# Kernel tuning notes

Hardware: AMD Instinct MI355X
Metric: run time of the kernel (lower is better)

## Reference

```python
import jax, jax.numpy as jnp
from jax import lax
import numpy as np

B, T, I, H, C = 32, 256, 128, 128, 100


def setup_inputs() -> dict:
    key = jax.random.key(0)
    ks = jax.random.split(key, 9)
    s = 1.0 / np.sqrt(H)  # PyTorch LSTMCell init range
    inp = {
        "x": jax.random.normal(ks[0], (B, T, I), dtype=jnp.float32),
        "w_ih": jax.random.uniform(ks[1], (4 * H, I), jnp.float32, -s, s),
        "b_ih": jax.random.uniform(ks[2], (4 * H,), jnp.float32, -s, s),
        "w_hh": jax.random.uniform(ks[3], (4 * H, H), jnp.float32, -s, s),
        "b_hh": jax.random.uniform(ks[4], (4 * H,), jnp.float32, -s, s),
        # attention params: normal(mean=0, std=0.01) per the source
        "w1": 0.01 * jax.random.normal(ks[5], (2 * H, H), dtype=jnp.float32),
        "w2": 0.01 * jax.random.normal(ks[6], (H, 1), dtype=jnp.float32),
        "w_fc": jax.random.uniform(ks[7], (C, H), jnp.float32, -s, s),
        "b_fc": jax.random.uniform(ks[8], (C,), jnp.float32, -s, s),
    }
    return inp


def _forward(x, w_ih, b_ih, w_hh, b_hh, w1, w2, w_fc, b_fc):
    Bv, Tv, _ = x.shape
    Hv = w_hh.shape[1]
    h0 = jnp.zeros((Bv, Hv), x.dtype)
    c0 = jnp.zeros((Bv, Hv), x.dtype)
    # memory buffer: slot 0 holds the initial zero hidden state (as in the
    # torch code, h_old starts as h_t=0); slots 1..T filled as we go.
    # Unwritten (future) slots are zero, so their attn contribution
    # attn_w * h_old is exactly zero -> no mask needed, matching the
    # growing-memory semantics of the original loop.
    mem0 = jnp.zeros((Bv, Tv + 1, Hv), x.dtype)
    attn0 = jnp.zeros((Bv, Hv), x.dtype)

    def step(carry, inp):
        h, c, mem, _ = carry
        x_t, i = inp
        # PyTorch LSTMCell: gate order i, f, g, o
        gates = x_t @ w_ih.T + b_ih + h @ w_hh.T + b_hh
        ig, fg, gg, og = jnp.split(gates, 4, axis=-1)
        c = jax.nn.sigmoid(fg) * c + jax.nn.sigmoid(ig) * jnp.tanh(gg)
        h = jax.nn.sigmoid(og) * jnp.tanh(c)
        # additive attention scores over the memory (NO softmax in source)
        h_rep = jnp.broadcast_to(h[:, None, :], mem.shape)  # [B, T+1, H]
        cat = jnp.concatenate([h_rep, mem], axis=-1)        # [B, T+1, 2H]
        s = jnp.tanh(cat @ w1) @ w2                          # [B, T+1, 1]
        attn_c = jnp.sum(s * mem, axis=1)                    # [B, H]
        mem = mem.at[:, i + 1, :].set(h)  # append h_t to memory
        return (h, c, mem, attn_c), None

    xs = (jnp.transpose(x, (1, 0, 2)), jnp.arange(Tv))
    (h, c, mem, attn_c), _ = lax.scan(step, (h0, c0, mem0, attn0), xs)
    return (h + attn_c) @ w_fc.T + b_fc


def reference(x, w_ih, b_ih, w_hh, b_hh, w1, w2, w_fc, b_fc):
    return _forward(x, w_ih, b_ih, w_hh, b_hh, w1, w2, w_fc, b_fc)
```

## Files before the change

kernel.cpp:

```cpp
#include <hip/hip_runtime.h>
#include <hip/hip_bf16.h>


#define Bsz 32
#define Tsz 256
#define Isz 128
#define Hsz 128
#define Csz 100
#define G4H 512

__device__ __forceinline__ float2 pk_fma(float2 a, float2 b, float2 c) {
    float2 d;
    asm("v_pk_fma_f32 %0, %1, %2, %3" : "=v"(d) : "v"(a), "v"(b), "v"(c));
    return d;
}
__device__ __forceinline__ float quad_rsum(float x) {
    int t = __builtin_amdgcn_update_dpp(0, __float_as_int(x), 0xB1, 0xF, 0xF, true);
    x += __int_as_float(t);
    t = __builtin_amdgcn_update_dpp(0, __float_as_int(x), 0x4E, 0xF, 0xF, true);
    x += __int_as_float(t);
    return x;
}
__device__ __forceinline__ float rcpf(float x) { return __builtin_amdgcn_rcpf(x); }
__device__ __forceinline__ float sigm_n(float x) { return rcpf(1.0f + __expf(-x)); }
__device__ __forceinline__ float tanh_n(float x) {
    float ax = fabsf(x);
    float e = __expf(-2.0f * ax);
    float t = (1.0f - e) * rcpf(1.0f + e);
    return copysignf(t, x);
}
__device__ __forceinline__ float tanh_s(float x) { return tanh_n(x); }

__global__ __launch_bounds__(256) void prep_kernel(
    const float* __restrict__ w_ih, const float* __restrict__ b_ih,
    const float* __restrict__ w_hh, const float* __restrict__ b_hh,
    float* __restrict__ wih_t, float* __restrict__ whh_pk, float* __restrict__ bias) {
    int idx = blockIdx.x * blockDim.x + threadIdx.x;
    if (idx < G4H * Isz) {
        int j = idx >> 7;
        int k = idx & 127;
        wih_t[k * G4H + j] = w_ih[idx];

        int j4  = idx & 3;
        int q   = (idx >> 2) & 3;
        int d   = (idx >> 4) & 127;
        int gi  = (idx >> 11) & 3;
        int kk4 = (idx >> 13) & 7;
        whh_pk[idx] = w_hh[(size_t)((gi << 7) + d) * 128 + (q << 5) + (kk4 << 2) + j4];
    }
    if (idx < G4H) bias[idx] = b_ih[idx] + b_hh[idx];
}

#define GBK 16
#define GLD 132

__global__ __launch_bounds__(256) void gemm128(
    const float* __restrict__ A, const float* __restrict__ Bm,
    const float* __restrict__ bias, float* __restrict__ C,
    int M, int N, int K) {
    __shared__ float As[GBK][GLD];
    __shared__ float Bs[GBK][GLD];
    const int tid = threadIdx.x;
    const int bm = blockIdx.y * 128;
    const int bn = blockIdx.x * 128;
    const int tx = tid & 15, ty = tid >> 4;
    float acc[8][8] = {};

    const int ar = tid >> 2;
    const int ac = (tid & 3) * 4;
    const int br = tid >> 5;
    const int bc = (tid & 31) * 4;

    for (int k0 = 0; k0 < K; k0 += GBK) {
        #pragma unroll
        for (int h = 0; h < 2; ++h) {
            int r = ar + 64 * h;
            float4 v = *(const float4*)(A + (size_t)(bm + r) * K + k0 + ac);
            As[ac + 0][r] = v.x;
            As[ac + 1][r] = v.y;
            As[ac + 2][r] = v.z;
            As[ac + 3][r] = v.w;
        }
        #pragma unroll
        for (int h = 0; h < 2; ++h) {
            int kr = br + 8 * h;
            float4 v = *(const float4*)(Bm + (size_t)(k0 + kr) * N + bn + bc);
            *(float4*)&Bs[kr][bc] = v;
        }
        __syncthreads();
        #pragma unroll
        for (int kk = 0; kk < GBK; ++kk) {
            float a[8], b[8];
            *(float4*)&a[0] = *(const float4*)&As[kk][ty * 8];
            *(float4*)&a[4] = *(const float4*)&As[kk][ty * 8 + 4];
            *(float4*)&b[0] = *(const float4*)&Bs[kk][tx * 8];
            *(float4*)&b[4] = *(const float4*)&Bs[kk][tx * 8 + 4];
            #pragma unroll
            for (int i = 0; i < 8; ++i)
                #pragma unroll
                for (int j = 0; j < 8; ++j)
                    acc[i][j] = fmaf(a[i], b[j], acc[i][j]);
        }
        __syncthreads();
    }
    float bb[8];
    #pragma unroll
    for (int j = 0; j < 8; ++j) bb[j] = bias ? bias[bn + tx * 8 + j] : 0.0f;
    #pragma unroll
    for (int i = 0; i < 8; ++i) {
        int row = bm + ty * 8 + i;
        float4 v0, v1;
        v0.x = acc[i][0] + bb[0]; v0.y = acc[i][1] + bb[1];
        v0.z = acc[i][2] + bb[2]; v0.w = acc[i][3] + bb[3];
        v1.x = acc[i][4] + bb[4]; v1.y = acc[i][5] + bb[5];
        v1.z = acc[i][6] + bb[6]; v1.w = acc[i][7] + bb[7];
        *(float4*)(C + (size_t)row * N + bn + tx * 8) = v0;
        *(float4*)(C + (size_t)row * N + bn + tx * 8 + 4) = v1;
    }
}

#define BM 64
#define BN 64
#define BKt 64
#define LDP 68

__global__ __launch_bounds__(256) void gemm_tn(
    const float* __restrict__ A, const float* __restrict__ Bm,
    const float* __restrict__ bias, float* __restrict__ C,
    int M, int N, int K) {
    __shared__ float As[BKt][LDP];
    __shared__ float Bs[BKt][LDP];
    int tid = threadIdx.x;
    int bm = blockIdx.y * BM;
    int bn = blockIdx.x * BN;
    int tx = tid & 15, ty = tid >> 4;
    float acc[4][4] = {};

    int lr = tid >> 4;
    int lc = (tid & 15) * 4;

    for (int k0 = 0; k0 < K; k0 += BKt) {
        #pragma unroll
        for (int p = 0; p < 4; ++p) {
            int row = p * 16 + lr;
            float4 v = *(const float4*)(A + (size_t)(bm + row) * K + k0 + lc);
            As[lc + 0][row] = v.x;
            As[lc + 1][row] = v.y;
            As[lc + 2][row] = v.z;
            As[lc + 3][row] = v.w;
        }
        #pragma unroll
        for (int p = 0; p < 4; ++p) {
            int kr = p * 16 + lr;
            float4 v = *(const float4*)(Bm + (size_t)(k0 + kr) * N + bn + lc);
            *(float4*)&Bs[kr][lc] = v;
        }
        __syncthreads();
        #pragma unroll
        for (int kk = 0; kk < BKt; ++kk) {
            float4 a = *(const float4*)&As[kk][ty * 4];
            float4 b = *(const float4*)&Bs[kk][tx * 4];
            acc[0][0] = fmaf(a.x, b.x, acc[0][0]);
            acc[0][1] = fmaf(a.x, b.y, acc[0][1]);
            acc[0][2] = fmaf(a.x, b.z, acc[0][2]);
            acc[0][3] = fmaf(a.x, b.w, acc[0][3]);
            acc[1][0] = fmaf(a.y, b.x, acc[1][0]);
            acc[1][1] = fmaf(a.y, b.y, acc[1][1]);
            acc[1][2] = fmaf(a.y, b.z, acc[1][2]);
            acc[1][3] = fmaf(a.y, b.w, acc[1][3]);
            acc[2][0] = fmaf(a.z, b.x, acc[2][0]);
            acc[2][1] = fmaf(a.z, b.y, acc[2][1]);
            acc[2][2] = fmaf(a.z, b.z, acc[2][2]);
            acc[2][3] = fmaf(a.z, b.w, acc[2][3]);
            acc[3][0] = fmaf(a.w, b.x, acc[3][0]);
            acc[3][1] = fmaf(a.w, b.y, acc[3][1]);
            acc[3][2] = fmaf(a.w, b.z, acc[3][2]);
            acc[3][3] = fmaf(a.w, b.w, acc[3][3]);
        }
        __syncthreads();
    }
    float bb[4] = {0.f, 0.f, 0.f, 0.f};
    if (bias) {
        bb[0] = bias[bn + tx * 4 + 0];
        bb[1] = bias[bn + tx * 4 + 1];
        bb[2] = bias[bn + tx * 4 + 2];
        bb[3] = bias[bn + tx * 4 + 3];
    }
    #pragma unroll
    for (int i = 0; i < 4; ++i) {
        int row = bm + ty * 4 + i;
        float4 v;
        v.x = acc[i][0] + bb[0];
        v.y = acc[i][1] + bb[1];
        v.z = acc[i][2] + bb[2];
        v.w = acc[i][3] + bb[3];
        *(float4*)(C + (size_t)row * N + bn + tx * 4) = v;
    }
}

#define HPAD(k) ((k) + 8 * ((k) >> 5))

__global__ __launch_bounds__(512, 2) void lstm_seq(
    const float* __restrict__ G, const float* __restrict__ whh_pk,
    float* __restrict__ H_all) {
    const int b = blockIdx.x;
    const int tid = threadIdx.x;
    const int d = tid >> 2;
    const int q = tid & 3;

    __shared__ float h_s[2][160];
    __shared__ float ring[8][Hsz];

    float2 w2v[4][16];
    {
        const float4* wp = (const float4*)whh_pk;
        #pragma unroll
        for (int kk4 = 0; kk4 < 8; ++kk4)
            #pragma unroll
            for (int gi = 0; gi < 4; ++gi) {
                float4 v = wp[((kk4 * 4 + gi) * 128 + d) * 4 + q];
                w2v[gi][kk4 * 2]     = make_float2(v.x, v.y);
                w2v[gi][kk4 * 2 + 1] = make_float2(v.z, v.w);
            }
    }

    if (tid < 320) ((float*)h_s)[tid] = 0.0f;
    float c = 0.0f;
    __syncthreads();

    const float* Gq = G + (size_t)b * Tsz * G4H + q * 128 + d;
    float* Hb = H_all + (size_t)b * Tsz * Hsz;

    const int fr = tid >> 6;
    const int fc = (tid * 2) & 127;

    float gval = Gq[0];
    int cur = 0;
    for (int t = 0; t < Tsz; ++t) {
        const int tn = (t < Tsz - 1) ? t + 1 : t;
        float ngval = Gq[(size_t)tn * G4H];

        float2 accA[4], accB[4];
        #pragma unroll
        for (int gi = 0; gi < 4; ++gi) {
            accA[gi] = make_float2(q == gi ? gval : 0.f, 0.f);
            accB[gi] = make_float2(0.f, 0.f);
        }
        const float4* hb4 = (const float4*)&h_s[cur][q * 40];
        #pragma unroll
        for (int kk4 = 0; kk4 < 8; ++kk4) {
            float4 h4 = hb4[kk4];
            float2 hA = make_float2(h4.x, h4.y);
            float2 hB = make_float2(h4.z, h4.w);
            accA[0] = pk_fma(hA, w2v[0][2 * kk4], accA[0]);
            accA[1] = pk_fma(hA, w2v[1][2 * kk4], accA[1]);
            accA[2] = pk_fma(hA, w2v[2][2 * kk4], accA[2]);
            accA[3] = pk_fma(hA, w2v[3][2 * kk4], accA[3]);
            accB[0] = pk_fma(hB, w2v[0][2 * kk4 + 1], accB[0]);
            accB[1] = pk_fma(hB, w2v[1][2 * kk4 + 1], accB[1]);
            accB[2] = pk_fma(hB, w2v[2][2 * kk4 + 1], accB[2]);
            accB[3] = pk_fma(hB, w2v[3][2 * kk4 + 1], accB[3]);
        }
        float a0 = quad_rsum(accA[0].x + accA[0].y + accB[0].x + accB[0].y);
        float a1 = quad_rsum(accA[1].x + accA[1].y + accB[1].x + accB[1].y);
        float a2 = quad_rsum(accA[2].x + accA[2].y + accB[2].x + accB[2].y);
        float a3 = quad_rsum(accA[3].x + accA[3].y + accB[3].x + accB[3].y);

        float iv = sigm_n(a0);
        float fv = sigm_n(a1);
        float gv = tanh_n(a2);
        float ov = sigm_n(a3);
        c = fv * c + iv * gv;
        float h = ov * tanh_n(c);

        int nxt = cur ^ 1;
        if (q == 0) {
            h_s[nxt][HPAD(d)] = h;
            ring[t & 7][d] = h;
        }
        gval = ngval;
        __syncthreads();
        cur = nxt;

        if ((t & 7) == 7) {
            float2 v = *(const float2*)&ring[fr][fc];
            *(float2*)&Hb[(size_t)(t - 7 + fr) * Hsz + fc] = v;
        }
    }
}

__global__ __launch_bounds__(256) void attn_out(
    const float* __restrict__ H_all, const float* __restrict__ KV,
    const float* __restrict__ w1, const float* __restrict__ w2,
    const float* __restrict__ w_fc, const float* __restrict__ b_fc,
    float* __restrict__ out) {
    int b = blockIdx.x;
    int tid = threadIdx.x;
    __shared__ float hT[Hsz];
    __shared__ float q_s[Hsz];
    __shared__ float w2s[Hsz];
    __shared__ float s_s[Tsz];
    __shared__ float r2[2][Hsz];
    __shared__ float r_s[Hsz];

    const float* Hb = H_all + (size_t)b * Tsz * Hsz;
    const float* KVb = KV + (size_t)b * Tsz * Hsz;

    if (tid < Hsz) {
        hT[tid] = Hb[255 * Hsz + tid];
        w2s[tid] = w2[tid];
    }
    __syncthreads();
    if (tid < Hsz) {
        float acc = 0.f;
        #pragma unroll 8
        for (int k = 0; k < Hsz; ++k) acc = fmaf(hT[k], w1[k * Hsz + tid], acc);
        q_s[tid] = acc;
    }
    __syncthreads();

    const int qd = tid >> 2, ql = tid & 3;
    #pragma unroll
    for (int jj = 0; jj < 4; ++jj) {
        int j = qd + jj * 64;
        float p = 0.f;
        if (j < 255) {
            const float* kv = KVb + (size_t)j * Hsz + ql * 32;
            const float* qs = q_s + ql * 32;
            const float* wv = w2s + ql * 32;
            #pragma unroll 8
            for (int k = 0; k < 32; ++k)
                p = fmaf(tanh_s(qs[k] + kv[k]), wv[k], p);
        }
        p = quad_rsum(p);
        if (ql == 0 && j < 255) s_s[j] = p;
    }
    __syncthreads();

    {
        int dd = tid & 127, half = tid >> 7;
        int j0 = half * 128, je = half ? 255 : 128;
        float acc = 0.f;
        #pragma unroll 4
        for (int j = j0; j < je; ++j) acc = fmaf(s_s[j], Hb[(size_t)j * Hsz + dd], acc);
        r2[half][dd] = acc;
    }
    __syncthreads();
    if (tid < Hsz) r_s[tid] = hT[tid] + r2[0][tid] + r2[1][tid];
    __syncthreads();

    {
        int o = tid >> 1, half = tid & 1;
        float acc = 0.f;
        if (o < Csz) {
            const float* wr = w_fc + (size_t)o * Hsz + half * 64;
            const float* rr = r_s + half * 64;
            #pragma unroll 8
            for (int k = 0; k < 64; ++k) acc = fmaf(rr[k], wr[k], acc);
        }
        acc += __shfl_xor(acc, 1);
        if (half == 0 && o < Csz) out[b * Csz + o] = acc + b_fc[o];
    }
}

extern "C" void kernel_launch(void* const* d_in, const int* in_sizes, int n_in,
                              void* d_out, int out_size, void* d_ws, size_t ws_size,
                              hipStream_t stream) {
    const float* x    = (const float*)d_in[0];
    const float* w_ih = (const float*)d_in[1];
    const float* b_ih = (const float*)d_in[2];
    const float* w_hh = (const float*)d_in[3];
    const float* b_hh = (const float*)d_in[4];
    const float* w1   = (const float*)d_in[5];
    const float* w2   = (const float*)d_in[6];
    const float* w_fc = (const float*)d_in[7];
    const float* b_fc = (const float*)d_in[8];

    float* ws = (float*)d_ws;
    float* wih_t  = ws;
    float* whh_pk = wih_t + 65536;
    float* bias   = whh_pk + 65536;
    float* G      = bias + 512;
    float* H_all  = G + 4194304;
    float* KV     = H_all + 1048576;

    prep_kernel<<<256, 256, 0, stream>>>(w_ih, b_ih, w_hh, b_hh, wih_t, whh_pk, bias);

    dim3 g1(G4H / 128, (Bsz * Tsz) / 128);
    gemm128<<<g1, 256, 0, stream>>>(x, wih_t, bias, G, Bsz * Tsz, G4H, Isz);

    lstm_seq<<<Bsz, 512, 0, stream>>>(G, whh_pk, H_all);

    dim3 g2(Hsz / BN, (Bsz * Tsz) / BM);
    gemm_tn<<<g2, 256, 0, stream>>>(H_all, w1 + Hsz * Hsz, nullptr, KV, Bsz * Tsz, Hsz, Hsz);

    attn_out<<<Bsz, 256, 0, stream>>>(H_all, KV, w1, w2, w_fc, b_fc, (float*)d_out);
}
```

Measured before the change: 345.5 us.

## Add producer/consumer warp specialization to LSTM recurrence kernel

Grows the LSTM block from 8 to 10 wavefronts. One extra wave prefetches the precomputed input-gate rows for the next 8 timesteps into a double-buffered LDS ring, and another writes finished hidden states back to global memory. The 8 compute waves now read gate values from LDS and no longer issue global loads or stores on the serial critical path. In exchange the block is larger, launch bounds allow only one block per CU, and LDS use goes up.

```diff
diff --git a/kernel.cpp b/kernel.cpp
--- a/kernel.cpp
+++ b/kernel.cpp
@@ -199,20 +199,27 @@
 }
 
 #define HPAD(k) ((k) + 8 * ((k) >> 5))
-
-__global__ __launch_bounds__(512, 2) void lstm_seq(
+#define LSTMT 640
+
+__global__ __launch_bounds__(LSTMT, 1) void lstm_seq(
     const float* __restrict__ G, const float* __restrict__ whh_pk,
     float* __restrict__ H_all) {
     const int b = blockIdx.x;
     const int tid = threadIdx.x;
+    const int wav = tid >> 6;
+    const int lane = tid & 63;
     const int d = tid >> 2;
     const int q = tid & 3;
 
     __shared__ float h_s[2][160];
-    __shared__ float ring[8][Hsz];
+    __shared__ float gring[2][8][G4H];
+    __shared__ float ring[2][8][Hsz];
+
+    const float* Gb = G + (size_t)b * Tsz * G4H;
+    float* Hb = H_all + (size_t)b * Tsz * Hsz;
 
     float2 w2v[4][16];
-    {
+    if (wav < 8) {
         const float4* wp = (const float4*)whh_pk;
         #pragma unroll
         for (int kk4 = 0; kk4 < 8; ++kk4)
@@ -224,68 +231,87 @@
             }
     }
 
+    for (int i4 = tid; i4 < 1024; i4 += LSTMT)
+        ((float4*)&gring[0][0][0])[i4] = ((const float4*)Gb)[i4];
     if (tid < 320) ((float*)h_s)[tid] = 0.0f;
     float c = 0.0f;
     __syncthreads();
 
-    const float* Gq = G + (size_t)b * Tsz * G4H + q * 128 + d;
-    float* Hb = H_all + (size_t)b * Tsz * Hsz;
-
-    const int fr = tid >> 6;
-    const int fc = (tid * 2) & 127;
-
-    float gval = Gq[0];
     int cur = 0;
     for (int t = 0; t < Tsz; ++t) {
-        const int tn = (t < Tsz - 1) ? t + 1 : t;
-        float ngval = Gq[(size_t)tn * G4H];
-
-        float2 accA[4], accB[4];
-        #pragma unroll
-        for (int gi = 0; gi < 4; ++gi) {
-            accA[gi] = make_float2(q == gi ? gval : 0.f, 0.f);
-            accB[gi] = make_float2(0.f, 0.f);
-        }
-        const float4* hb4 = (const float4*)&h_s[cur][q * 40];
-        #pragma unroll
-        for (int kk4 = 0; kk4 < 8; ++kk4) {
-            float4 h4 = hb4[kk4];
-            float2 hA = make_float2(h4.x, h4.y);
-            float2 hB = make_float2(h4.z, h4.w);
-            accA[0] = pk_fma(hA, w2v[0][2 * kk4], accA[0]);
-            accA[1] = pk_fma(hA, w2v[1][2 * kk4], accA[1]);
-            accA[2] = pk_fma(hA, w2v[2][2 * kk4], accA[2]);
-            accA[3] = pk_fma(hA, w2v[3][2 * kk4], accA[3]);
-            accB[0] = pk_fma(hB, w2v[0][2 * kk4 + 1], accB[0]);
-            accB[1] = pk_fma(hB, w2v[1][2 * kk4 + 1], accB[1]);
-            accB[2] = pk_fma(hB, w2v[2][2 * kk4 + 1], accB[2]);
-            accB[3] = pk_fma(hB, w2v[3][2 * kk4 + 1], accB[3]);
-        }
-        float a0 = quad_rsum(accA[0].x + accA[0].y + accB[0].x + accB[0].y);
-        float a1 = quad_rsum(accA[1].x + accA[1].y + accB[1].x + accB[1].y);
-        float a2 = quad_rsum(accA[2].x + accA[2].y + accB[2].x + accB[2].y);
-        float a3 = quad_rsum(accA[3].x + accA[3].y + accB[3].x + accB[3].y);
-
-        float iv = sigm_n(a0);
-        float fv = sigm_n(a1);
-        float gv = tanh_n(a2);
-        float ov = sigm_n(a3);
-        c = fv * c + iv * gv;
-        float h = ov * tanh_n(c);
-
-        int nxt = cur ^ 1;
-        if (q == 0) {
-            h_s[nxt][HPAD(d)] = h;
-            ring[t & 7][d] = h;
-        }
-        gval = ngval;
+        const int chunk = t >> 3;
+        const int ph = t & 7;
+        const int par = chunk & 1;
+
+        if (wav < 8) {
+            float gval = gring[par][ph][q * 128 + d];
+            float2 accA[4], accB[4];
+            #pragma unroll
+            for (int gi = 0; gi < 4; ++gi) {
+                accA[gi] = make_float2(q == gi ? gval : 0.f, 0.f);
+                accB[gi] = make_float2(0.f, 0.f);
+            }
+            const float4* hb4 = (const float4*)&h_s[cur][q * 40];
+            #pragma unroll
+            for (int kk4 = 0; kk4 < 8; ++kk4) {
+                float4 h4 = hb4[kk4];
+                float2 hA = make_float2(h4.x, h4.y);
+                float2 hB = make_float2(h4.z, h4.w);
+                accA[0] = pk_fma(hA, w2v[0][2 * kk4], accA[0]);
+                accA[1] = pk_fma(hA, w2v[1][2 * kk4], accA[1]);
+                accA[2] = pk_fma(hA, w2v[2][2 * kk4], accA[2]);
+                accA[3] = pk_fma(hA, w2v[3][2 * kk4], accA[3]);
+                accB[0] = pk_fma(hB, w2v[0][2 * kk4 + 1], accB[0]);
+                accB[1] = pk_fma(hB, w2v[1][2 * kk4 + 1], accB[1]);
+                accB[2] = pk_fma(hB, w2v[2][2 * kk4 + 1], accB[2]);
+                accB[3] = pk_fma(hB, w2v[3][2 * kk4 + 1], accB[3]);
+            }
+            float a0 = quad_rsum(accA[0].x + accA[0].y + accB[0].x + accB[0].y);
+            float a1 = quad_rsum(accA[1].x + accA[1].y + accB[1].x + accB[1].y);
+            float a2 = quad_rsum(accA[2].x + accA[2].y + accB[2].x + accB[2].y);
+            float a3 = quad_rsum(accA[3].x + accA[3].y + accB[3].x + accB[3].y);
+
+            float iv = sigm_n(a0);
+            float fv = sigm_n(a1);
+            float gv = tanh_n(a2);
+            float ov = sigm_n(a3);
+            c = fv * c + iv * gv;
+            float h = ov * tanh_n(c);
+
+            if (q == 0) {
+                h_s[cur ^ 1][HPAD(d)] = h;
+                ring[par][ph][d] = h;
+            }
+            cur ^= 1;
+        } else if (wav == 8) {
+            if (ph == 4 && chunk < 31) {
+                const float4* src = (const float4*)(Gb + (size_t)(chunk + 1) * 4096);
+                float4* dst = (float4*)&gring[(chunk + 1) & 1][0][0];
+                float4 tmp[16];
+                #pragma unroll
+                for (int s = 0; s < 16; ++s) tmp[s] = src[lane + 64 * s];
+                #pragma unroll
+                for (int s = 0; s < 16; ++s) dst[lane + 64 * s] = tmp[s];
+            }
+        } else {
+            if (ph == 0 && chunk > 0) {
+                const float4* rs = (const float4*)&ring[(chunk - 1) & 1][0][0];
+                float4* dsg = (float4*)(Hb + (size_t)(chunk - 1) * 1024);
+                float4 tmp[4];
+                #pragma unroll
+                for (int s = 0; s < 4; ++s) tmp[s] = rs[lane + 64 * s];
+                #pragma unroll
+                for (int s = 0; s < 4; ++s) dsg[lane + 64 * s] = tmp[s];
+            }
+        }
         __syncthreads();
-        cur = nxt;
-
-        if ((t & 7) == 7) {
-            float2 v = *(const float2*)&ring[fr][fc];
-            *(float2*)&Hb[(size_t)(t - 7 + fr) * Hsz + fc] = v;
-        }
+    }
+
+    if (wav == 9) {
+        const float4* rs = (const float4*)&ring[1][0][0];
+        float4* dsg = (float4*)(Hb + (size_t)31 * 1024);
+        #pragma unroll
+        for (int s = 0; s < 4; ++s) dsg[lane + 64 * s] = rs[lane + 64 * s];
     }
 }
 
@@ -389,7 +415,7 @@
     dim3 g1(G4H / 128, (Bsz * Tsz) / 128);
     gemm128<<<g1, 256, 0, stream>>>(x, wih_t, bias, G, Bsz * Tsz, G4H, Isz);
 
-    lstm_seq<<<Bsz, 512, 0, stream>>>(G, whh_pk, H_all);
+    lstm_seq<<<Bsz, LSTMT, 0, stream>>>(G, whh_pk, H_all);
 
     dim3 g2(Hsz / BN, (Bsz * Tsz) / BM);
     gemm_tn<<<g2, 256, 0, stream>>>(H_all, w1 + Hsz * Hsz, nullptr, KV, Bsz * Tsz, Hsz, Hsz);
```

After: 456.3 us. 1.32x slower.

## Batch G prefetch per 8 steps, keep h in registers, reuse gemm128 for KV

Applied to the files above, without the earlier changes.

The LSTM recurrence is restructured into 8-step chunks. Each chunk loads all 8 G values up front, and each thread keeps its h values in a register ring that it writes directly to global memory, replacing the shared-memory ring and its cooperative store. The separate 64x64 gemm_tn kernel is removed and the KV projection now uses the existing 128x128 gemm128 kernel. The aim is to cut per-step global-load latency and shared-memory traffic on the serial critical path. In exchange it uses more registers and makes uncoalesced strided stores from the q==0 lanes.

```diff
diff --git a/kernel.cpp b/kernel.cpp
--- a/kernel.cpp
+++ b/kernel.cpp
@@ -119,85 +119,6 @@
     }
 }
 
-#define BM 64
-#define BN 64
-#define BKt 64
-#define LDP 68
-
-__global__ __launch_bounds__(256) void gemm_tn(
-    const float* __restrict__ A, const float* __restrict__ Bm,
-    const float* __restrict__ bias, float* __restrict__ C,
-    int M, int N, int K) {
-    __shared__ float As[BKt][LDP];
-    __shared__ float Bs[BKt][LDP];
-    int tid = threadIdx.x;
-    int bm = blockIdx.y * BM;
-    int bn = blockIdx.x * BN;
-    int tx = tid & 15, ty = tid >> 4;
-    float acc[4][4] = {};
-
-    int lr = tid >> 4;
-    int lc = (tid & 15) * 4;
-
-    for (int k0 = 0; k0 < K; k0 += BKt) {
-        #pragma unroll
-        for (int p = 0; p < 4; ++p) {
-            int row = p * 16 + lr;
-            float4 v = *(const float4*)(A + (size_t)(bm + row) * K + k0 + lc);
-            As[lc + 0][row] = v.x;
-            As[lc + 1][row] = v.y;
-            As[lc + 2][row] = v.z;
-            As[lc + 3][row] = v.w;
-        }
-        #pragma unroll
-        for (int p = 0; p < 4; ++p) {
-            int kr = p * 16 + lr;
-            float4 v = *(const float4*)(Bm + (size_t)(k0 + kr) * N + bn + lc);
-            *(float4*)&Bs[kr][lc] = v;
-        }
-        __syncthreads();
-        #pragma unroll
-        for (int kk = 0; kk < BKt; ++kk) {
-            float4 a = *(const float4*)&As[kk][ty * 4];
-            float4 b = *(const float4*)&Bs[kk][tx * 4];
-            acc[0][0] = fmaf(a.x, b.x, acc[0][0]);
-            acc[0][1] = fmaf(a.x, b.y, acc[0][1]);
-            acc[0][2] = fmaf(a.x, b.z, acc[0][2]);
-            acc[0][3] = fmaf(a.x, b.w, acc[0][3]);
-            acc[1][0] = fmaf(a.y, b.x, acc[1][0]);
-            acc[1][1] = fmaf(a.y, b.y, acc[1][1]);
-            acc[1][2] = fmaf(a.y, b.z, acc[1][2]);
-            acc[1][3] = fmaf(a.y, b.w, acc[1][3]);
-            acc[2][0] = fmaf(a.z, b.x, acc[2][0]);
-            acc[2][1] = fmaf(a.z, b.y, acc[2][1]);
-            acc[2][2] = fmaf(a.z, b.z, acc[2][2]);
-            acc[2][3] = fmaf(a.z, b.w, acc[2][3]);
-            acc[3][0] = fmaf(a.w, b.x, acc[3][0]);
-            acc[3][1] = fmaf(a.w, b.y, acc[3][1]);
-            acc[3][2] = fmaf(a.w, b.z, acc[3][2]);
-            acc[3][3] = fmaf(a.w, b.w, acc[3][3]);
-        }
-        __syncthreads();
-    }
-    float bb[4] = {0.f, 0.f, 0.f, 0.f};
-    if (bias) {
-        bb[0] = bias[bn + tx * 4 + 0];
-        bb[1] = bias[bn + tx * 4 + 1];
-        bb[2] = bias[bn + tx * 4 + 2];
-        bb[3] = bias[bn + tx * 4 + 3];
-    }
-    #pragma unroll
-    for (int i = 0; i < 4; ++i) {
-        int row = bm + ty * 4 + i;
-        float4 v;
-        v.x = acc[i][0] + bb[0];
-        v.y = acc[i][1] + bb[1];
-        v.z = acc[i][2] + bb[2];
-        v.w = acc[i][3] + bb[3];
-        *(float4*)(C + (size_t)row * N + bn + tx * 4) = v;
-    }
-}
-
 #define HPAD(k) ((k) + 8 * ((k) >> 5))
 
 __global__ __launch_bounds__(512, 2) void lstm_seq(
@@ -209,7 +130,6 @@
     const int q = tid & 3;
 
     __shared__ float h_s[2][160];
-    __shared__ float ring[8][Hsz];
 
     float2 w2v[4][16];
     {
@@ -229,63 +149,65 @@
     __syncthreads();
 
     const float* Gq = G + (size_t)b * Tsz * G4H + q * 128 + d;
-    float* Hb = H_all + (size_t)b * Tsz * Hsz;
-
-    const int fr = tid >> 6;
-    const int fc = (tid * 2) & 127;
-
-    float gval = Gq[0];
+    float* Hst = H_all + (size_t)b * Tsz * Hsz + d;
+
+    float hring[8];
     int cur = 0;
-    for (int t = 0; t < Tsz; ++t) {
-        const int tn = (t < Tsz - 1) ? t + 1 : t;
-        float ngval = Gq[(size_t)tn * G4H];
-
-        float2 accA[4], accB[4];
-        #pragma unroll
-        for (int gi = 0; gi < 4; ++gi) {
-            accA[gi] = make_float2(q == gi ? gval : 0.f, 0.f);
-            accB[gi] = make_float2(0.f, 0.f);
-        }
-        const float4* hb4 = (const float4*)&h_s[cur][q * 40];
-        #pragma unroll
-        for (int kk4 = 0; kk4 < 8; ++kk4) {
-            float4 h4 = hb4[kk4];
-            float2 hA = make_float2(h4.x, h4.y);
-            float2 hB = make_float2(h4.z, h4.w);
-            accA[0] = pk_fma(hA, w2v[0][2 * kk4], accA[0]);
-            accA[1] = pk_fma(hA, w2v[1][2 * kk4], accA[1]);
-            accA[2] = pk_fma(hA, w2v[2][2 * kk4], accA[2]);
-            accA[3] = pk_fma(hA, w2v[3][2 * kk4], accA[3]);
-            accB[0] = pk_fma(hB, w2v[0][2 * kk4 + 1], accB[0]);
-            accB[1] = pk_fma(hB, w2v[1][2 * kk4 + 1], accB[1]);
-            accB[2] = pk_fma(hB, w2v[2][2 * kk4 + 1], accB[2]);
-            accB[3] = pk_fma(hB, w2v[3][2 * kk4 + 1], accB[3]);
-        }
-        float a0 = quad_rsum(accA[0].x + accA[0].y + accB[0].x + accB[0].y);
-        float a1 = quad_rsum(accA[1].x + accA[1].y + accB[1].x + accB[1].y);
-        float a2 = quad_rsum(accA[2].x + accA[2].y + accB[2].x + accB[2].y);
-        float a3 = quad_rsum(accA[3].x + accA[3].y + accB[3].x + accB[3].y);
-
-        float iv = sigm_n(a0);
-        float fv = sigm_n(a1);
-        float gv = tanh_n(a2);
-        float ov = sigm_n(a3);
-        c = fv * c + iv * gv;
-        float h = ov * tanh_n(c);
-
-        int nxt = cur ^ 1;
-        if (q == 0) {
-            h_s[nxt][HPAD(d)] = h;
-            ring[t & 7][d] = h;
-        }
-        gval = ngval;
-        __syncthreads();
-        cur = nxt;
-
-        if ((t & 7) == 7) {
-            float2 v = *(const float2*)&ring[fr][fc];
-            *(float2*)&Hb[(size_t)(t - 7 + fr) * Hsz + fc] = v;
-        }
+
+    for (int t0 = 0; t0 < Tsz; t0 += 8) {
+        float gb[8];
+        #pragma unroll
+        for (int s = 0; s < 8; ++s) gb[s] = Gq[(size_t)(t0 + s) * G4H];
+        if (t0 > 0 && q == 0) {
+            #pragma unroll
+            for (int s = 0; s < 8; ++s) Hst[(size_t)(t0 - 8 + s) * Hsz] = hring[s];
+        }
+
+        #pragma unroll
+        for (int ph = 0; ph < 8; ++ph) {
+            float gval = gb[ph];
+            float2 accA[4], accB[4];
+            #pragma unroll
+            for (int gi = 0; gi < 4; ++gi) {
+                accA[gi] = make_float2(q == gi ? gval : 0.f, 0.f);
+                accB[gi] = make_float2(0.f, 0.f);
+            }
+            const float4* hb4 = (const float4*)&h_s[cur][q * 40];
+            #pragma unroll
+            for (int kk4 = 0; kk4 < 8; ++kk4) {
+                float4 h4 = hb4[kk4];
+                float2 hA = make_float2(h4.x, h4.y);
+                float2 hB = make_float2(h4.z, h4.w);
+                accA[0] = pk_fma(hA, w2v[0][2 * kk4], accA[0]);
+                accA[1] = pk_fma(hA, w2v[1][2 * kk4], accA[1]);
+                accA[2] = pk_fma(hA, w2v[2][2 * kk4], accA[2]);
+                accA[3] = pk_fma(hA, w2v[3][2 * kk4], accA[3]);
+                accB[0] = pk_fma(hB, w2v[0][2 * kk4 + 1], accB[0]);
+                accB[1] = pk_fma(hB, w2v[1][2 * kk4 + 1], accB[1]);
+                accB[2] = pk_fma(hB, w2v[2][2 * kk4 + 1], accB[2]);
+                accB[3] = pk_fma(hB, w2v[3][2 * kk4 + 1], accB[3]);
+            }
+            float a0 = quad_rsum(accA[0].x + accA[0].y + accB[0].x + accB[0].y);
+            float a1 = quad_rsum(accA[1].x + accA[1].y + accB[1].x + accB[1].y);
+            float a2 = quad_rsum(accA[2].x + accA[2].y + accB[2].x + accB[2].y);
+            float a3 = quad_rsum(accA[3].x + accA[3].y + accB[3].x + accB[3].y);
+
+            float iv = sigm_n(a0);
+            float fv = sigm_n(a1);
+            float gv = tanh_n(a2);
+            float ov = sigm_n(a3);
+            c = fv * c + iv * gv;
+            float h = ov * tanh_n(c);
+
+            if (q == 0) h_s[cur ^ 1][HPAD(d)] = h;
+            hring[ph] = h;
+            __syncthreads();
+            cur ^= 1;
+        }
+    }
+    if (q == 0) {
+        #pragma unroll
+        for (int s = 0; s < 8; ++s) Hst[(size_t)(248 + s) * Hsz] = hring[s];
     }
 }
 
@@ -391,8 +313,8 @@
 
     lstm_seq<<<Bsz, 512, 0, stream>>>(G, whh_pk, H_all);
 
-    dim3 g2(Hsz / BN, (Bsz * Tsz) / BM);
-    gemm_tn<<<g2, 256, 0, stream>>>(H_all, w1 + Hsz * Hsz, nullptr, KV, Bsz * Tsz, Hsz, Hsz);
+    dim3 g2(Hsz / 128, (Bsz * Tsz) / 128);
+    gemm128<<<g2, 256, 0, stream>>>(H_all, w1 + Hsz * Hsz, nullptr, KV, Bsz * Tsz, Hsz, Hsz);
 
     attn_out<<<Bsz, 256, 0, stream>>>(H_all, KV, w1, w2, w_fc, b_fc, (float*)d_out);
 }
```

Result: no change. 341.1 us (-1.3%).
